# Optimization experiments

Hardware: AMD Instinct MI355X
Metric: run time of the kernel (lower is better)

Reference implementation:

```python
import jax, jax.numpy as jnp
import numpy as np

N_HEADS = 4
WINDOW = 606      # causal sliding-window width
K_PEEK = 606      # phy-output peek length (y_phy is zeros -> zeros anyway)
K_PEEK_TRUE = 30  # true-measurement peek length
LN_EPS = 1e-5


def _layernorm(x, g, b):
    m = jnp.mean(x, axis=-1, keepdims=True)
    v = jnp.var(x, axis=-1, keepdims=True)
    return (x - m) / jnp.sqrt(v + LN_EPS) * g + b


def _pos_encoding(T, d):
    pos = jnp.arange(T, dtype=jnp.float32)[:, None]
    div = jnp.exp(jnp.arange(0, d, 2, dtype=jnp.float32) * (-jnp.log(10000.0) / d))
    pe = jnp.zeros((T, d), jnp.float32)
    pe = pe.at[:, 0::2].set(jnp.sin(pos * div))
    pe = pe.at[:, 1::2].set(jnp.cos(pos * div))
    return pe


def setup_inputs() -> dict:
    key = jax.random.key(0)
    ks = iter(jax.random.split(key, 40))
    B, T, u_dim, y_dim, z_dim, h, L = 4, 2048, 8, 8, 16, 512, 4
    dff = 4 * h
    w = lambda shape: jax.random.normal(next(ks), shape, jnp.float32) * 0.02
    return {
        'u': jax.random.normal(next(ks), (B, u_dim, T), jnp.float32),
        'y': jax.random.normal(next(ks), (B, y_dim, T), jnp.float32),
        'W_in': w((u_dim + 2 * y_dim, h)), 'b_in': jnp.zeros((h,), jnp.float32),
        'qkv_w': w((L, h, 3 * h)), 'qkv_b': jnp.zeros((L, 3 * h), jnp.float32),
        'out_w': w((L, h, h)), 'out_b': jnp.zeros((L, h), jnp.float32),
        'ff1_w': w((L, h, dff)), 'ff1_b': jnp.zeros((L, dff), jnp.float32),
        'ff2_w': w((L, dff, h)), 'ff2_b': jnp.zeros((L, h), jnp.float32),
        'ln1_g': jnp.ones((L, h), jnp.float32), 'ln1_b': jnp.zeros((L, h), jnp.float32),
        'ln2_g': jnp.ones((L, h), jnp.float32), 'ln2_b': jnp.zeros((L, h), jnp.float32),
        'lnf_g': jnp.ones((h,), jnp.float32), 'lnf_b': jnp.zeros((h,), jnp.float32),
        'xm1_w': w((h, h)), 'xm1_b': jnp.zeros((h,), jnp.float32),
        'xm2_w': w((h, z_dim)), 'xm2_b': jnp.zeros((z_dim,), jnp.float32),
        'me1_w': w((z_dim, h)), 'me1_b': jnp.zeros((h,), jnp.float32),
        'me2_w': w((h, h)), 'me2_b': jnp.zeros((h,), jnp.float32),
        'me3_w': w((h, y_dim)), 'me3_b': jnp.zeros((y_dim,), jnp.float32),
    }


def _forward(u, y, W_in, b_in, qkv_w, qkv_b, out_w, out_b, ff1_w, ff1_b,
             ff2_w, ff2_b, ln1_g, ln1_b, ln2_g, ln2_b, lnf_g, lnf_b,
             xm1_w, xm1_b, xm2_w, xm2_b, me1_w, me1_b, me2_w, me2_b, me3_w, me3_b):
    B, y_dim, T = y.shape
    u_t = jnp.transpose(u, (0, 2, 1))          # [B,T,u_dim]
    y_t = jnp.transpose(y, (0, 2, 1))          # [B,T,y_dim]
    # phy rollout produces zeros (zero-init MODEL_PHY surrogate) -> y_aug = 0
    y_aug = jnp.zeros((B, T, y_dim), jnp.float32)
    k_true = min(K_PEEK_TRUE, T)
    y_aug_true = jnp.concatenate(
        [y_t[:, :k_true, :], jnp.zeros((B, T - k_true, y_dim), jnp.float32)], axis=1)
    u_aug = jnp.concatenate([u_t, y_aug, y_aug_true], axis=2)  # [B,T,u+2y]

    h = W_in.shape[1]
    x = u_aug @ W_in + b_in + _pos_encoding(T, h)[None]        # [B,T,h]

    # causal sliding-window mask: row i attends to j in [i-WINDOW+1, i]
    i = jnp.arange(T)[:, None]
    j = jnp.arange(T)[None, :]
    allowed = (j <= i) & (j > i - WINDOW)                      # [T,T] bool

    dh = h // N_HEADS
    L = qkv_w.shape[0]
    for l in range(L):
        qkv = x @ qkv_w[l] + qkv_b[l]                          # [B,T,3h]
        q, k, v = jnp.split(qkv, 3, axis=-1)
        q = q.reshape(B, T, N_HEADS, dh)
        k = k.reshape(B, T, N_HEADS, dh)
        v = v.reshape(B, T, N_HEADS, dh)
        scores = jnp.einsum('bqhd,bkhd->bhqk', q, k) / jnp.sqrt(jnp.float32(dh))
        scores = jnp.where(allowed[None, None], scores, jnp.float32(-1e30))
        probs = jax.nn.softmax(scores, axis=-1)
        attn = jnp.einsum('bhqk,bkhd->bqhd', probs, v).reshape(B, T, h)
        attn = attn @ out_w[l] + out_b[l]
        x = _layernorm(x + attn, ln1_g[l], ln1_b[l])           # post-norm
        ff = jax.nn.gelu(x @ ff1_w[l] + ff1_b[l], approximate=False) @ ff2_w[l] + ff2_b[l]
        x = _layernorm(x + ff, ln2_g[l], ln2_b[l])
    x = _layernorm(x, lnf_g, lnf_b)

    x_mean = jax.nn.gelu(x @ xm1_w + xm1_b, approximate=False) @ xm2_w + xm2_b
    hme = jax.nn.gelu(x_mean @ me1_w + me1_b, approximate=False)
    hme = jax.nn.gelu(hme @ me2_w + me2_b, approximate=False)
    y_hat = hme @ me3_w + me3_b                                # [B,T,y_dim]

    loss = jnp.sum((y_hat - y_t) ** 2)                         # lamba_smooth = 0
    return loss


def reference(u, y, W_in, b_in, qkv_w, qkv_b, out_w, out_b, ff1_w, ff1_b,
              ff2_w, ff2_b, ln1_g, ln1_b, ln2_g, ln2_b, lnf_g, lnf_b,
              xm1_w, xm1_b, xm2_w, xm2_b, me1_w, me1_b, me2_w, me2_b, me3_w, me3_b):
    return _forward(u, y, W_in, b_in, qkv_w, qkv_b, out_w, out_b, ff1_w, ff1_b,
                    ff2_w, ff2_b, ln1_g, ln1_b, ln2_g, ln2_b, lnf_g, lnf_b,
                    xm1_w, xm1_b, xm2_w, xm2_b, me1_w, me1_b, me2_w, me2_b, me3_w, me3_b)
```

## Files before the change

### kernel.cpp

```cpp
#include <hip/hip_runtime.h>
#include <cstdint>
#include <cstddef>

#define TT 2048
#define BB 4
#define HDIM 512
#define NH 4
#define LAYERS 4
#define WINDOW 606

#define PLANE_QK 4194304ull
#define PLANE_X  4194304ull
#define PLANE_FF 16777216ull

typedef __attribute__((ext_vector_type(8))) short bf16x8s;
typedef __attribute__((ext_vector_type(4))) float f32x4;

__device__ __forceinline__ float wred_sum(float v) {
#pragma unroll
  for (int off = 32; off; off >>= 1) v += __shfl_xor(v, off, 64);
  return v;
}
__device__ __forceinline__ float gelu_exact(float x) {
  return 0.5f * x * (1.0f + erff(x * 0.70710678118654752f));
}
__device__ __forceinline__ ushort bf16_rne(float v) {
  uint32_t u = __float_as_uint(v);
  u += 0x7FFFu + ((u >> 16) & 1u);
  return (ushort)(u >> 16);
}
__device__ __forceinline__ void split3(float v, ushort& h, ushort& l) {
  h = bf16_rne(v);
  const float hf = __uint_as_float(((uint32_t)h) << 16);
  l = bf16_rne(v - hf);
}
__device__ __forceinline__ void gld_lds16(const void* g, void* l) {
  __builtin_amdgcn_global_load_lds(
      (const __attribute__((address_space(1))) uint32_t*)g,
      (__attribute__((address_space(3))) uint32_t*)l, 16, 0, 0);
}

__global__ __launch_bounds__(256) void embed_kernel(
    const float* __restrict__ u, const float* __restrict__ y,
    const float* __restrict__ W_in, const float* __restrict__ b_in,
    float* __restrict__ X, ushort* __restrict__ xp) {
  const int row = blockIdx.x;
  const int b = row >> 11;
  const int t = row & 2047;
  const int tid = threadIdx.x;
  __shared__ float ua[24];
  if (tid < 8)       ua[tid] = u[((b << 3) + tid) * TT + t];
  else if (tid < 16) ua[tid] = 0.0f;
  else if (tid < 24) ua[tid] = (t < 30) ? y[((b << 3) + (tid - 16)) * TT + t] : 0.0f;
  __syncthreads();
#pragma unroll
  for (int c0 = 0; c0 < 2; ++c0) {
    const int c = c0 * 256 + tid;
    float s = b_in[c];
#pragma unroll
    for (int k = 0; k < 24; ++k) s += ua[k] * W_in[k * HDIM + c];
    const float dv = expf(-0.0179889460337f * (float)(c & ~1));
    const float arg = (float)t * dv;
    s += (c & 1) ? cosf(arg) : sinf(arg);
    X[(size_t)row * HDIM + c] = s;
    ushort h, l2; split3(s, h, l2);
    xp[(size_t)row * HDIM + c] = h;
    xp[PLANE_X + (size_t)row * HDIM + c] = l2;
  }
}

__device__ __forceinline__ void pack_tile(float (*tile)[33],
    const float* __restrict__ W, ushort* __restrict__ Wp,
    int K, int N, int bk, int bn, int tid) {
  const int i0 = tid >> 5, j = tid & 31;
#pragma unroll
  for (int i = 0; i < 4; ++i) {
    const int kk = i0 + i * 8;
    tile[kk][j] = W[(size_t)(bk + kk) * N + bn + j];
  }
  __syncthreads();
  const size_t NK = (size_t)N * K;
#pragma unroll
  for (int i = 0; i < 4; ++i) {
    const int nn = i0 + i * 8;
    const float v = tile[j][nn];
    ushort h, l2; split3(v, h, l2);
    ushort* base = Wp + (size_t)(bn + nn) * K + bk + j;
    base[0] = h; base[NK] = l2;
  }
}

__global__ __launch_bounds__(256) void packL_kernel(
    const float* __restrict__ qkvw, const float* __restrict__ outw,
    const float* __restrict__ ff1w, ushort* __restrict__ Wp) {
  __shared__ float tile[32][33];
  int i = blockIdx.x;
  if (i < 768) {
    pack_tile(tile, qkvw, Wp, 512, 1536, (i & 15) * 32, (i >> 4) * 32, threadIdx.x);
  } else if (i < 1024) {
    i -= 768;
    pack_tile(tile, outw, Wp + 1572864, 512, 512, (i & 15) * 32, (i >> 4) * 32, threadIdx.x);
  } else {
    i -= 1024;
    pack_tile(tile, ff1w, Wp + 2097152, 512, 2048, (i & 15) * 32, (i >> 4) * 32, threadIdx.x);
  }
}

__global__ __launch_bounds__(256) void packF_kernel(
    const float* __restrict__ ff2w, ushort* __restrict__ Wp) {
  __shared__ float tile[32][33];
  const int i = blockIdx.x;
  pack_tile(tile, ff2w, Wp, 2048, 512, (i & 63) * 32, (i >> 6) * 32, threadIdx.x);
}

__global__ __launch_bounds__(256) void packH_kernel(
    const float* __restrict__ xm1w, const float* __restrict__ me2w,
    ushort* __restrict__ Wp) {
  __shared__ float tile[32][33];
  int i = blockIdx.x;
  if (i < 256) pack_tile(tile, xm1w, Wp, 512, 512, (i & 15) * 32, (i >> 4) * 32, threadIdx.x);
  else { i -= 256; pack_tile(tile, me2w, Wp + 524288, 512, 512, (i & 15) * 32, (i >> 4) * 32, threadIdx.x); }
}

template <int ACT, int OUTMODE, int RM>
__global__ __launch_bounds__(256) void gemm_mfma(
    const ushort* __restrict__ Ah, const ushort* __restrict__ Al,
    const ushort* __restrict__ Bh, const ushort* __restrict__ Bl,
    const float* __restrict__ bias,
    float* __restrict__ C, ushort* __restrict__ Cp, size_t cplane,
    ushort* __restrict__ Wq, int M, int N, int K, int nbn) {
  constexpr int IA = RM / 32;
  constexpr int JA = RM / 64;
  __shared__ ushort AlsH[RM * 32];
  __shared__ ushort AlsL[RM * 32];
  __shared__ ushort BlsH[4096];
  __shared__ ushort BlsL[4096];
  __shared__ float biasL[128];
  const int tid = threadIdx.x;
  const int cpx = (int)gridDim.x >> 3;
  const int bid = blockIdx.x;
  const int lid = (bid & 7) * cpx + (bid >> 3);
  const int bn = (lid % nbn) * 128;
  const int bm = (lid / nbn) * RM;
  const int w = tid >> 6, ln = tid & 63;
  const int wr = (w >> 1) * (RM / 2), wc = (w & 1) * 64;
  const int c = ln & 15, g = ln >> 4;
  if (tid < 128) biasL[tid] = bias[bn + tid];
  const int srow = tid >> 2;
  const int scol = (tid & 3) * 8;

  f32x4 acc[IA][4] = {};
  for (int k0 = 0; k0 < K; k0 += 32) {
#pragma unroll
    for (int j = 0; j < JA; ++j) {
      const size_t ga = (size_t)(bm + j * 64 + srow) * K + k0 + scol;
      const int off = j * 4096 + tid * 16;
      gld_lds16(Ah + ga, (char*)AlsH + off);
      gld_lds16(Al + ga, (char*)AlsL + off);
    }
#pragma unroll
    for (int j = 0; j < 2; ++j) {
      const size_t gb = (size_t)(bn + j * 64 + srow) * K + k0 + scol;
      const int off = j * 4096 + tid * 16;
      gld_lds16(Bh + gb, (char*)BlsH + off);
      gld_lds16(Bl + gb, (char*)BlsL + off);
    }
    __syncthreads();
    bf16x8s fah[IA], fal[IA], fbh[4], fbl[4];
#pragma unroll
    for (int i = 0; i < IA; ++i) {
      const int ao = (wr + i * 16 + c) * 32 + g * 8;
      fah[i] = *(const bf16x8s*)&AlsH[ao];
      fal[i] = *(const bf16x8s*)&AlsL[ao];
    }
#pragma unroll
    for (int i = 0; i < 4; ++i) {
      const int bo = (wc + i * 16 + c) * 32 + g * 8;
      fbh[i] = *(const bf16x8s*)&BlsH[bo];
      fbl[i] = *(const bf16x8s*)&BlsL[bo];
    }
#pragma unroll
    for (int i = 0; i < IA; ++i)
#pragma unroll
      for (int j = 0; j < 4; ++j) {
        acc[i][j] = __builtin_amdgcn_mfma_f32_16x16x32_bf16(fah[i], fbh[j], acc[i][j], 0, 0, 0);
        acc[i][j] = __builtin_amdgcn_mfma_f32_16x16x32_bf16(fal[i], fbh[j], acc[i][j], 0, 0, 0);
        acc[i][j] = __builtin_amdgcn_mfma_f32_16x16x32_bf16(fah[i], fbl[j], acc[i][j], 0, 0, 0);
      }
    __syncthreads();
  }
  const float qscale = 0.08838834764831845f * 1.44269504088896341f;
#pragma unroll
  for (int i = 0; i < IA; ++i) {
    const int grow0 = bm + wr + i * 16 + g * 4;
#pragma unroll
    for (int j = 0; j < 4; ++j) {
      const int gcol = bn + wc + j * 16 + c;
      const float bv = biasL[wc + j * 16 + c];
      if (OUTMODE == 2) {
        const int bq = grow0 >> 11, tl = grow0 & 2047;
        if (bn < 512) {
          const int hh = gcol >> 7, d = gcol & 127;
          ushort* dst = Wq + ((size_t)(bq * NH + hh) * TT + tl) * 128 + d;
#pragma unroll
          for (int r = 0; r < 4; ++r) {
            ushort h, l2; split3((acc[i][j][r] + bv) * qscale, h, l2);
            dst[(size_t)r * 128] = h;
            dst[PLANE_QK + (size_t)r * 128] = l2;
          }
        } else if (bn < 1024) {
          const int hh = (gcol - 512) >> 7, d = gcol & 127;
          ushort* dst = Wq + 2 * PLANE_QK + ((size_t)(bq * NH + hh) * TT + tl) * 128 + d;
#pragma unroll
          for (int r = 0; r < 4; ++r) {
            ushort h, l2; split3(acc[i][j][r] + bv, h, l2);
            dst[(size_t)r * 128] = h;
            dst[PLANE_QK + (size_t)r * 128] = l2;
          }
        } else {
          const int hh = (gcol - 1024) >> 7, d = gcol & 127;
          ushort4 h4, l4;
          split3(acc[i][j][0] + bv, h4.x, l4.x);
          split3(acc[i][j][1] + bv, h4.y, l4.y);
          split3(acc[i][j][2] + bv, h4.z, l4.z);
          split3(acc[i][j][3] + bv, h4.w, l4.w);
          ushort* dst = Wq + 4 * PLANE_QK + ((size_t)(bq * NH + hh) * 128 + d) * TT + tl;
          *(ushort4*)dst = h4;
          *(ushort4*)(dst + PLANE_QK) = l4;
        }
      } else {
#pragma unroll
        for (int r = 0; r < 4; ++r) {
          float v = acc[i][j][r] + bv;
          if (ACT) v = gelu_exact(v);
          if (OUTMODE == 1) {
            ushort h, l2; split3(v, h, l2);
            ushort* base = Cp + (size_t)(grow0 + r) * N + gcol;
            base[0] = h; base[cplane] = l2;
          } else {
            C[(size_t)(grow0 + r) * N + gcol] = v;
          }
        }
      }
    }
  }
}

template <int ACT, int PACK>
__global__ __launch_bounds__(256) void gemm_bias(
    const float* __restrict__ A, const float* __restrict__ B,
    const float* __restrict__ bias, float* __restrict__ C,
    ushort* __restrict__ Cp, size_t cplane, int M, int N, int K) {
  __shared__ float As[16][132];
  __shared__ float Bs[16][64];
  const int bm = blockIdx.y * 128;
  const int bn = blockIdx.x * 64;
  const int tid = threadIdx.x;
  const int tx = tid & 15, ty = tid >> 4;
  float acc[8][4] = {};
  for (int k0 = 0; k0 < K; k0 += 16) {
#pragma unroll
    for (int i = 0; i < 8; ++i) {
      const int idx = i * 256 + tid;
      const int m = idx >> 4, k = idx & 15;
      As[k][m] = A[(size_t)(bm + m) * K + k0 + k];
    }
#pragma unroll
    for (int i = 0; i < 4; ++i) {
      const int idx = i * 256 + tid;
      const int k = idx >> 6, n = idx & 63;
      Bs[k][n] = (bn + n < N) ? B[(size_t)(k0 + k) * N + bn + n] : 0.0f;
    }
    __syncthreads();
#pragma unroll
    for (int kk = 0; kk < 16; ++kk) {
      float a[8], bb[4];
#pragma unroll
      for (int i = 0; i < 8; ++i) a[i] = As[kk][ty * 8 + i];
#pragma unroll
      for (int j = 0; j < 4; ++j) bb[j] = Bs[kk][tx * 4 + j];
#pragma unroll
      for (int i = 0; i < 8; ++i)
#pragma unroll
        for (int j = 0; j < 4; ++j) acc[i][j] += a[i] * bb[j];
    }
    __syncthreads();
  }
#pragma unroll
  for (int i = 0; i < 8; ++i) {
    const int m = bm + ty * 8 + i;
#pragma unroll
    for (int j = 0; j < 4; ++j) {
      const int n = bn + tx * 4 + j;
      if (n < N) {
        float v = acc[i][j] + bias[n];
        if (ACT) v = gelu_exact(v);
        if (PACK) {
          ushort h, l2; split3(v, h, l2);
          ushort* base = Cp + (size_t)m * N + n;
          base[0] = h; base[cplane] = l2;
        } else {
          C[(size_t)m * N + n] = v;
        }
      }
    }
  }
}

__global__ __launch_bounds__(256) void attn_mfma(
    const ushort* __restrict__ QKVp, ushort* __restrict__ atp) {
  const int bid = blockIdx.x;
  const int lid = (bid & 7) * 128 + (bid >> 3);
  const int q0 = (lid & 63) * 32;
  const int bh = lid >> 6;
  const int b = bh >> 2, hh = bh & 3;
  const int tid = threadIdx.x;
  const int w = tid >> 6, lane = tid & 63;
  const int c = lane & 15, g = lane >> 4;
  const int wr = w >> 1, wc = w & 1;

  __shared__ ushort Ph[32][40], Pl[32][40];
  __shared__ float wmax[2][32], wsum[2][32];
  __shared__ float mrow[2][32], lrow[2][32];

  const ushort* Qh = QKVp;
  const ushort* Ql = QKVp + PLANE_QK;
  const ushort* Kh = QKVp + 2 * PLANE_QK;
  const ushort* Kl = QKVp + 3 * PLANE_QK;
  const ushort* Vh = QKVp + 4 * PLANE_QK;
  const ushort* Vl = QKVp + 5 * PLANE_QK;

  const size_t qkbase = (size_t)bh * TT * 128;
  const size_t vtbase = (size_t)bh * 128 * TT;

  bf16x8s qh[4], ql[4];
  {
    const ushort* qr = Qh + qkbase + (size_t)(q0 + wr * 16 + c) * 128 + g * 8;
    const ushort* qr2 = Ql + qkbase + (size_t)(q0 + wr * 16 + c) * 128 + g * 8;
#pragma unroll
    for (int kc = 0; kc < 4; ++kc) {
      qh[kc] = *(const bf16x8s*)(qr + kc * 32);
      ql[kc] = *(const bf16x8s*)(qr2 + kc * 32);
    }
  }

  if (tid < 32) { mrow[0][tid] = -1e30f; lrow[0][tid] = 0.0f; }
  __syncthreads();

  f32x4 oacc[2][2] = {};
  int par = 0;
  int lo_ = q0 - (WINDOW - 1); if (lo_ < 0) lo_ = 0;
  const int k_first = lo_ & ~31;
  const int qg = q0 + wr * 16 + c;
  const int qrow = wr * 16 + c;

  for (int k0 = k_first; k0 <= q0; k0 += 32) {
    const bf16x8s vh0 = *(const bf16x8s*)(Vh + vtbase + (size_t)(w * 32 + c) * TT + k0 + g * 8);
    const bf16x8s vh1 = *(const bf16x8s*)(Vh + vtbase + (size_t)(w * 32 + 16 + c) * TT + k0 + g * 8);
    const bf16x8s vl0 = *(const bf16x8s*)(Vl + vtbase + (size_t)(w * 32 + c) * TT + k0 + g * 8);
    const bf16x8s vl1 = *(const bf16x8s*)(Vl + vtbase + (size_t)(w * 32 + 16 + c) * TT + k0 + g * 8);

    f32x4 sacc = {};
    {
      const ushort* kr = Kh + qkbase + (size_t)(k0 + wc * 16 + c) * 128 + g * 8;
      const ushort* kr2 = Kl + qkbase + (size_t)(k0 + wc * 16 + c) * 128 + g * 8;
      bf16x8s kh[4], kl[4];
#pragma unroll
      for (int kc = 0; kc < 4; ++kc) {
        kh[kc] = *(const bf16x8s*)(kr + kc * 32);
        kl[kc] = *(const bf16x8s*)(kr2 + kc * 32);
      }
#pragma unroll
      for (int kc = 0; kc < 4; ++kc)
        sacc = __builtin_amdgcn_mfma_f32_16x16x32_bf16(kh[kc], qh[kc], sacc, 0, 0, 0);
#pragma unroll
      for (int kc = 0; kc < 4; ++kc)
        sacc = __builtin_amdgcn_mfma_f32_16x16x32_bf16(kl[kc], qh[kc], sacc, 0, 0, 0);
#pragma unroll
      for (int kc = 0; kc < 4; ++kc)
        sacc = __builtin_amdgcn_mfma_f32_16x16x32_bf16(kh[kc], ql[kc], sacc, 0, 0, 0);
    }
    float s[4];
    float m4 = -1e30f;
#pragma unroll
    for (int r = 0; r < 4; ++r) {
      const int kj = k0 + wc * 16 + g * 4 + r;
      const bool ok = (kj <= qg) && (kj > qg - WINDOW);
      s[r] = ok ? sacc[r] : -1e30f;
      m4 = fmaxf(m4, s[r]);
    }
    m4 = fmaxf(m4, __shfl_xor(m4, 16, 64));
    m4 = fmaxf(m4, __shfl_xor(m4, 32, 64));
    if (lane < 16) wmax[wc][qrow] = m4;
    __syncthreads();

    {
      const float mt = fmaxf(wmax[0][qrow], wmax[1][qrow]);
      const float mn = fmaxf(mrow[par][qrow], mt);
      float pv[4];
      float ps = 0.0f;
#pragma unroll
      for (int r = 0; r < 4; ++r) {
        pv[r] = (s[r] > -1e29f) ? exp2f(s[r] - mn) : 0.0f;
        ps += pv[r];
      }
      ps += __shfl_xor(ps, 16, 64);
      ps += __shfl_xor(ps, 32, 64);
      if (lane < 16) wsum[wc][qrow] = ps;
      ushort4 h4, l4;
      split3(pv[0], h4.x, l4.x); split3(pv[1], h4.y, l4.y);
      split3(pv[2], h4.z, l4.z); split3(pv[3], h4.w, l4.w);
      *(ushort4*)&Ph[qrow][wc * 16 + g * 4] = h4;
      *(ushort4*)&Pl[qrow][wc * 16 + g * 4] = l4;
    }
    __syncthreads();

    if (tid < 32) {
      const float mt = fmaxf(wmax[0][tid], wmax[1][tid]);
      const float mo = mrow[par][tid];
      const float mn = fmaxf(mo, mt);
      mrow[par ^ 1][tid] = mn;
      lrow[par ^ 1][tid] = lrow[par][tid] * exp2f(mo - mn) + wsum[0][tid] + wsum[1][tid];
    }
#pragma unroll
    for (int rh = 0; rh < 2; ++rh) {
      float sc[4];
#pragma unroll
      for (int r = 0; r < 4; ++r) {
        const int row = rh * 16 + g * 4 + r;
        const float mt = fmaxf(wmax[0][row], wmax[1][row]);
        const float mo = mrow[par][row];
        sc[r] = exp2f(mo - fmaxf(mo, mt));
      }
#pragma unroll
      for (int jt = 0; jt < 2; ++jt)
#pragma unroll
        for (int r = 0; r < 4; ++r) oacc[rh][jt][r] *= sc[r];
      const bf16x8s pah = *(const bf16x8s*)&Ph[rh * 16 + c][g * 8];
      const bf16x8s pal = *(const bf16x8s*)&Pl[rh * 16 + c][g * 8];
      oacc[rh][0] = __builtin_amdgcn_mfma_f32_16x16x32_bf16(pah, vh0, oacc[rh][0], 0, 0, 0);
      oacc[rh][0] = __builtin_amdgcn_mfma_f32_16x16x32_bf16(pal, vh0, oacc[rh][0], 0, 0, 0);
      oacc[rh][0] = __builtin_amdgcn_mfma_f32_16x16x32_bf16(pah, vl0, oacc[rh][0], 0, 0, 0);
      oacc[rh][1] = __builtin_amdgcn_mfma_f32_16x16x32_bf16(pah, vh1, oacc[rh][1], 0, 0, 0);
      oacc[rh][1] = __builtin_amdgcn_mfma_f32_16x16x32_bf16(pal, vh1, oacc[rh][1], 0, 0, 0);
      oacc[rh][1] = __builtin_amdgcn_mfma_f32_16x16x32_bf16(pah, vl1, oacc[rh][1], 0, 0, 0);
    }
    __syncthreads();
    par ^= 1;
  }

#pragma unroll
  for (int rh = 0; rh < 2; ++rh) {
#pragma unroll
    for (int r = 0; r < 4; ++r) {
      const int row = rh * 16 + g * 4 + r;
      const float li = 1.0f / lrow[par][row];
      const int qgo = q0 + row;
      ushort* base = atp + (size_t)(b * TT + qgo) * HDIM + hh * 128;
#pragma unroll
      for (int jt = 0; jt < 2; ++jt) {
        const int d = w * 32 + jt * 16 + c;
        ushort h, l2; split3(oacc[rh][jt][r] * li, h, l2);
        base[d] = h;
        base[PLANE_X + d] = l2;
      }
    }
  }
}

template <int HAS_RES>
__global__ __launch_bounds__(128) void ln_kernel(
    const float* __restrict__ x, const float* __restrict__ r,
    const float* __restrict__ g, const float* __restrict__ be,
    float* __restrict__ out, ushort* __restrict__ xp) {
  const int row = blockIdx.x, tid = threadIdx.x;
  float4 v = ((const float4*)(x + (size_t)row * HDIM))[tid];
  if (HAS_RES) {
    const float4 rv = ((const float4*)(r + (size_t)row * HDIM))[tid];
    v.x += rv.x; v.y += rv.y; v.z += rv.z; v.w += rv.w;
  }
  __shared__ float red[2];
  float s = v.x + v.y + v.z + v.w;
  s = wred_sum(s);
  if ((tid & 63) == 0) red[tid >> 6] = s;
  __syncthreads();
  const float mean = (red[0] + red[1]) * (1.0f / 512.0f);
  const float dx = v.x - mean, dy = v.y - mean, dz = v.z - mean, dw = v.w - mean;
  float s2 = dx * dx + dy * dy + dz * dz + dw * dw;
  __syncthreads();
  s2 = wred_sum(s2);
  if ((tid & 63) == 0) red[tid >> 6] = s2;
  __syncthreads();
  const float var = (red[0] + red[1]) * (1.0f / 512.0f);
  const float inv = 1.0f / sqrtf(var + 1e-5f);
  const float4 gv = ((const float4*)g)[tid];
  const float4 bv = ((const float4*)be)[tid];
  float4 o;
  o.x = dx * inv * gv.x + bv.x;
  o.y = dy * inv * gv.y + bv.y;
  o.z = dz * inv * gv.z + bv.z;
  o.w = dw * inv * gv.w + bv.w;
  ((float4*)(out + (size_t)row * HDIM))[tid] = o;
  ushort4 h4, l4;
  split3(o.x, h4.x, l4.x); split3(o.y, h4.y, l4.y);
  split3(o.z, h4.z, l4.z); split3(o.w, h4.w, l4.w);
  ushort* basep = xp + (size_t)row * HDIM + tid * 4;
  *(ushort4*)basep = h4;
  *(ushort4*)(basep + PLANE_X) = l4;
}

__global__ __launch_bounds__(256) void head_loss_kernel(
    const float* __restrict__ hme, const float* __restrict__ w3,
    const float* __restrict__ b3, const float* __restrict__ y,
    float* __restrict__ partials) {
  const int row = blockIdx.x;
  const int b = row >> 11, t = row & 2047;
  const int tid = threadIdx.x;
  __shared__ __align__(16) float hl[512];
  __shared__ float acc8[8];
  ((float2*)hl)[tid] = ((const float2*)(hme + (size_t)row * HDIM))[tid];
  __syncthreads();
  const int d = tid >> 5, l32 = tid & 31;
  float s = 0.0f;
  for (int k = l32; k < 512; k += 32) s += hl[k] * w3[k * 8 + d];
#pragma unroll
  for (int off = 16; off; off >>= 1) s += __shfl_xor(s, off, 64);
  if (l32 == 0) {
    const float yh = s + b3[d];
    const float diff = yh - y[((b << 3) + d) * TT + t];
    acc8[d] = diff * diff;
  }
  __syncthreads();
  if (tid == 0) {
    float tot = 0.0f;
#pragma unroll
    for (int i = 0; i < 8; ++i) tot += acc8[i];
    partials[row] = tot;
  }
}

__global__ __launch_bounds__(256) void reduce_kernel(
    const float* __restrict__ partials, float* __restrict__ out, int n) {
  float s = 0.0f;
  for (int i = threadIdx.x; i < n; i += 256) s += partials[i];
  s = wred_sum(s);
  __shared__ float red[4];
  if ((threadIdx.x & 63) == 0) red[threadIdx.x >> 6] = s;
  __syncthreads();
  if (threadIdx.x == 0) out[0] = red[0] + red[1] + red[2] + red[3];
}

extern "C" void kernel_launch(void* const* d_in, const int* in_sizes, int n_in,
                              void* d_out, int out_size, void* d_ws, size_t ws_size,
                              hipStream_t stream) {
  (void)in_sizes; (void)n_in; (void)out_size; (void)ws_size;
  const float* u     = (const float*)d_in[0];
  const float* y     = (const float*)d_in[1];
  const float* W_in  = (const float*)d_in[2];
  const float* b_in  = (const float*)d_in[3];
  const float* qkv_w = (const float*)d_in[4];
  const float* qkv_b = (const float*)d_in[5];
  const float* out_w = (const float*)d_in[6];
  const float* out_b = (const float*)d_in[7];
  const float* ff1_w = (const float*)d_in[8];
  const float* ff1_b = (const float*)d_in[9];
  const float* ff2_w = (const float*)d_in[10];
  const float* ff2_b = (const float*)d_in[11];
  const float* ln1_g = (const float*)d_in[12];
  const float* ln1_b = (const float*)d_in[13];
  const float* ln2_g = (const float*)d_in[14];
  const float* ln2_b = (const float*)d_in[15];
  const float* lnf_g = (const float*)d_in[16];
  const float* lnf_b = (const float*)d_in[17];
  const float* xm1_w = (const float*)d_in[18];
  const float* xm1_b = (const float*)d_in[19];
  const float* xm2_w = (const float*)d_in[20];
  const float* xm2_b = (const float*)d_in[21];
  const float* me1_w = (const float*)d_in[22];
  const float* me1_b = (const float*)d_in[23];
  const float* me2_w = (const float*)d_in[24];
  const float* me2_b = (const float*)d_in[25];
  const float* me3_w = (const float*)d_in[26];
  const float* me3_b = (const float*)d_in[27];

  const int M = BB * TT;
  char* ws = (char*)d_ws;
  float*  X    = (float*)(ws);
  float*  PRJ  = (float*)(ws + ((size_t)16 << 20));
  ushort* BIGp = (ushort*)(ws + ((size_t)32 << 20));
  ushort* PK1  = (ushort*)(ws + ((size_t)96 << 20));
  ushort* WSCR = (ushort*)(ws + ((size_t)112 << 20));
  float*  XM   = (float*)(ws + ((size_t)120 << 20));
  float*  PART = (float*)(ws + ((size_t)121 << 20));

  embed_kernel<<<M, 256, 0, stream>>>(u, y, W_in, b_in, X, PK1);

  for (int l = 0; l < LAYERS; ++l) {
    packL_kernel<<<2048, 256, 0, stream>>>(
        qkv_w + (size_t)l * 512 * 1536, out_w + (size_t)l * 512 * 512,
        ff1_w + (size_t)l * 512 * 2048, WSCR);
    gemm_mfma<0, 2, 128><<<768, 256, 0, stream>>>(
        PK1, PK1 + PLANE_X, WSCR, WSCR + 786432, qkv_b + l * 1536,
        nullptr, nullptr, 0, BIGp, M, 1536, 512, 12);
    attn_mfma<<<1024, 256, 0, stream>>>(BIGp, PK1);
    gemm_mfma<0, 0, 64><<<512, 256, 0, stream>>>(
        PK1, PK1 + PLANE_X, WSCR + 1572864, WSCR + 1835008, out_b + l * 512,
        PRJ, nullptr, 0, nullptr, M, 512, 512, 4);
    ln_kernel<1><<<M, 128, 0, stream>>>(X, PRJ, ln1_g + l * 512, ln1_b + l * 512, X, PK1);
    gemm_mfma<1, 1, 128><<<1024, 256, 0, stream>>>(
        PK1, PK1 + PLANE_X, WSCR + 2097152, WSCR + 3145728, ff1_b + l * 2048,
        nullptr, BIGp, PLANE_FF, nullptr, M, 2048, 512, 16);
    packF_kernel<<<1024, 256, 0, stream>>>(ff2_w + (size_t)l * 2048 * 512, WSCR);
    gemm_mfma<0, 0, 64><<<512, 256, 0, stream>>>(
        BIGp, BIGp + PLANE_FF, WSCR, WSCR + 1048576, ff2_b + l * 512,
        PRJ, nullptr, 0, nullptr, M, 512, 2048, 4);
    ln_kernel<1><<<M, 128, 0, stream>>>(X, PRJ, ln2_g + l * 512, ln2_b + l * 512, X, PK1);
  }
  ln_kernel<0><<<M, 128, 0, stream>>>(X, nullptr, lnf_g, lnf_b, X, PK1);

  packH_kernel<<<512, 256, 0, stream>>>(xm1_w, me2_w, WSCR);
  gemm_mfma<1, 0, 64><<<512, 256, 0, stream>>>(
      PK1, PK1 + PLANE_X, WSCR, WSCR + 262144, xm1_b,
      PRJ, nullptr, 0, nullptr, M, 512, 512, 4);
  gemm_bias<0, 0><<<dim3(1, 64), 256, 0, stream>>>(PRJ, xm2_w, xm2_b, XM, nullptr, 0, M, 16, 512);
  gemm_bias<1, 1><<<dim3(8, 64), 256, 0, stream>>>(XM, me1_w, me1_b, nullptr, PK1, PLANE_X, M, 512, 16);
  gemm_mfma<1, 0, 64><<<512, 256, 0, stream>>>(
      PK1, PK1 + PLANE_X, WSCR + 524288, WSCR + 786432, me2_b,
      PRJ, nullptr, 0, nullptr, M, 512, 512, 4);
  head_loss_kernel<<<M, 256, 0, stream>>>(PRJ, me3_w, me3_b, y, PART);
  reduce_kernel<<<1, 256, 0, stream>>>(PART, (float*)d_out, M);
}
```

Measured before the change: 1.854 ms.

## Process 64 keys per attention iteration and raise MFMA wave priority

The sliding-window attention loop now handles 64 keys per step instead of 32. It computes two score tiles side by side and widens the shared P buffers to 64 columns. This halves the number of per-iteration __syncthreads barriers and online-softmax rescale passes, and gives more independent MFMA chains to interleave. It also wraps the MFMA sections in s_setprio. The cost is higher register pressure and some extra masked work at window edges, since the start is now aligned to 64.

```diff
diff --git a/kernel.cpp b/kernel.cpp
--- a/kernel.cpp
+++ b/kernel.cpp
@@ -319,7 +319,7 @@
   const int c = lane & 15, g = lane >> 4;
   const int wr = w >> 1, wc = w & 1;
 
-  __shared__ ushort Ph[32][40], Pl[32][40];
+  __shared__ ushort Ph[32][72], Pl[32][72];
   __shared__ float wmax[2][32], wsum[2][32];
   __shared__ float mrow[2][32], lrow[2][32];
 
@@ -350,68 +350,92 @@
   f32x4 oacc[2][2] = {};
   int par = 0;
   int lo_ = q0 - (WINDOW - 1); if (lo_ < 0) lo_ = 0;
-  const int k_first = lo_ & ~31;
+  const int k_first = lo_ & ~63;
   const int qg = q0 + wr * 16 + c;
   const int qrow = wr * 16 + c;
 
-  for (int k0 = k_first; k0 <= q0; k0 += 32) {
-    const bf16x8s vh0 = *(const bf16x8s*)(Vh + vtbase + (size_t)(w * 32 + c) * TT + k0 + g * 8);
-    const bf16x8s vh1 = *(const bf16x8s*)(Vh + vtbase + (size_t)(w * 32 + 16 + c) * TT + k0 + g * 8);
-    const bf16x8s vl0 = *(const bf16x8s*)(Vl + vtbase + (size_t)(w * 32 + c) * TT + k0 + g * 8);
-    const bf16x8s vl1 = *(const bf16x8s*)(Vl + vtbase + (size_t)(w * 32 + 16 + c) * TT + k0 + g * 8);
-
-    f32x4 sacc = {};
+  for (int k0 = k_first; k0 < q0 + 32; k0 += 64) {
+    f32x4 sA = {}, sB = {};
     {
-      const ushort* kr = Kh + qkbase + (size_t)(k0 + wc * 16 + c) * 128 + g * 8;
-      const ushort* kr2 = Kl + qkbase + (size_t)(k0 + wc * 16 + c) * 128 + g * 8;
-      bf16x8s kh[4], kl[4];
+      const ushort* krA  = Kh + qkbase + (size_t)(k0 + wc * 16 + c) * 128 + g * 8;
+      const ushort* krA2 = Kl + qkbase + (size_t)(k0 + wc * 16 + c) * 128 + g * 8;
+      const ushort* krB  = Kh + qkbase + (size_t)(k0 + 32 + wc * 16 + c) * 128 + g * 8;
+      const ushort* krB2 = Kl + qkbase + (size_t)(k0 + 32 + wc * 16 + c) * 128 + g * 8;
+      bf16x8s kAh[4], kAl[4], kBh[4], kBl[4];
 #pragma unroll
       for (int kc = 0; kc < 4; ++kc) {
-        kh[kc] = *(const bf16x8s*)(kr + kc * 32);
-        kl[kc] = *(const bf16x8s*)(kr2 + kc * 32);
-      }
-#pragma unroll
-      for (int kc = 0; kc < 4; ++kc)
-        sacc = __builtin_amdgcn_mfma_f32_16x16x32_bf16(kh[kc], qh[kc], sacc, 0, 0, 0);
-#pragma unroll
-      for (int kc = 0; kc < 4; ++kc)
-        sacc = __builtin_amdgcn_mfma_f32_16x16x32_bf16(kl[kc], qh[kc], sacc, 0, 0, 0);
-#pragma unroll
-      for (int kc = 0; kc < 4; ++kc)
-        sacc = __builtin_amdgcn_mfma_f32_16x16x32_bf16(kh[kc], ql[kc], sacc, 0, 0, 0);
-    }
-    float s[4];
-    float m4 = -1e30f;
+        kAh[kc] = *(const bf16x8s*)(krA + kc * 32);
+        kAl[kc] = *(const bf16x8s*)(krA2 + kc * 32);
+        kBh[kc] = *(const bf16x8s*)(krB + kc * 32);
+        kBl[kc] = *(const bf16x8s*)(krB2 + kc * 32);
+      }
+      __builtin_amdgcn_s_setprio(1);
+#pragma unroll
+      for (int kc = 0; kc < 4; ++kc) {
+        sA = __builtin_amdgcn_mfma_f32_16x16x32_bf16(kAh[kc], qh[kc], sA, 0, 0, 0);
+        sB = __builtin_amdgcn_mfma_f32_16x16x32_bf16(kBh[kc], qh[kc], sB, 0, 0, 0);
+      }
+#pragma unroll
+      for (int kc = 0; kc < 4; ++kc) {
+        sA = __builtin_amdgcn_mfma_f32_16x16x32_bf16(kAl[kc], qh[kc], sA, 0, 0, 0);
+        sB = __builtin_amdgcn_mfma_f32_16x16x32_bf16(kBl[kc], qh[kc], sB, 0, 0, 0);
+      }
+#pragma unroll
+      for (int kc = 0; kc < 4; ++kc) {
+        sA = __builtin_amdgcn_mfma_f32_16x16x32_bf16(kAh[kc], ql[kc], sA, 0, 0, 0);
+        sB = __builtin_amdgcn_mfma_f32_16x16x32_bf16(kBh[kc], ql[kc], sB, 0, 0, 0);
+      }
+      __builtin_amdgcn_s_setprio(0);
+    }
+
+    bf16x8s vfh[2][2], vfl[2][2];
+#pragma unroll
+    for (int kh2 = 0; kh2 < 2; ++kh2)
+#pragma unroll
+      for (int jt = 0; jt < 2; ++jt) {
+        const size_t voff = vtbase + (size_t)(w * 32 + jt * 16 + c) * TT + k0 + kh2 * 32 + g * 8;
+        vfh[kh2][jt] = *(const bf16x8s*)(Vh + voff);
+        vfl[kh2][jt] = *(const bf16x8s*)(Vl + voff);
+      }
+
+    float e[8];
+    float mx = -1e30f;
 #pragma unroll
     for (int r = 0; r < 4; ++r) {
-      const int kj = k0 + wc * 16 + g * 4 + r;
-      const bool ok = (kj <= qg) && (kj > qg - WINDOW);
-      s[r] = ok ? sacc[r] : -1e30f;
-      m4 = fmaxf(m4, s[r]);
-    }
-    m4 = fmaxf(m4, __shfl_xor(m4, 16, 64));
-    m4 = fmaxf(m4, __shfl_xor(m4, 32, 64));
-    if (lane < 16) wmax[wc][qrow] = m4;
+      const int kjA = k0 + wc * 16 + 4 * g + r;
+      const int kjB = kjA + 32;
+      const bool okA = (kjA <= qg) && (kjA > qg - WINDOW);
+      const bool okB = (kjB <= qg) && (kjB > qg - WINDOW);
+      e[r]     = okA ? sA[r] : -1e30f;
+      e[4 + r] = okB ? sB[r] : -1e30f;
+      mx = fmaxf(mx, fmaxf(e[r], e[4 + r]));
+    }
+    mx = fmaxf(mx, __shfl_xor(mx, 16, 64));
+    mx = fmaxf(mx, __shfl_xor(mx, 32, 64));
+    if (lane < 16) wmax[wc][qrow] = mx;
     __syncthreads();
 
     {
       const float mt = fmaxf(wmax[0][qrow], wmax[1][qrow]);
       const float mn = fmaxf(mrow[par][qrow], mt);
-      float pv[4];
       float ps = 0.0f;
 #pragma unroll
-      for (int r = 0; r < 4; ++r) {
-        pv[r] = (s[r] > -1e29f) ? exp2f(s[r] - mn) : 0.0f;
-        ps += pv[r];
+      for (int i = 0; i < 8; ++i) {
+        e[i] = (e[i] > -1e29f) ? exp2f(e[i] - mn) : 0.0f;
+        ps += e[i];
       }
       ps += __shfl_xor(ps, 16, 64);
       ps += __shfl_xor(ps, 32, 64);
       if (lane < 16) wsum[wc][qrow] = ps;
-      ushort4 h4, l4;
-      split3(pv[0], h4.x, l4.x); split3(pv[1], h4.y, l4.y);
-      split3(pv[2], h4.z, l4.z); split3(pv[3], h4.w, l4.w);
-      *(ushort4*)&Ph[qrow][wc * 16 + g * 4] = h4;
-      *(ushort4*)&Pl[qrow][wc * 16 + g * 4] = l4;
+      ushort4 hA, lA, hB, lB;
+      split3(e[0], hA.x, lA.x); split3(e[1], hA.y, lA.y);
+      split3(e[2], hA.z, lA.z); split3(e[3], hA.w, lA.w);
+      split3(e[4], hB.x, lB.x); split3(e[5], hB.y, lB.y);
+      split3(e[6], hB.z, lB.z); split3(e[7], hB.w, lB.w);
+      *(ushort4*)&Ph[qrow][wc * 16 + 4 * g] = hA;
+      *(ushort4*)&Pl[qrow][wc * 16 + 4 * g] = lA;
+      *(ushort4*)&Ph[qrow][32 + wc * 16 + 4 * g] = hB;
+      *(ushort4*)&Pl[qrow][32 + wc * 16 + 4 * g] = lB;
     }
     __syncthreads();
 
@@ -436,14 +460,19 @@
       for (int jt = 0; jt < 2; ++jt)
 #pragma unroll
         for (int r = 0; r < 4; ++r) oacc[rh][jt][r] *= sc[r];
-      const bf16x8s pah = *(const bf16x8s*)&Ph[rh * 16 + c][g * 8];
-      const bf16x8s pal = *(const bf16x8s*)&Pl[rh * 16 + c][g * 8];
-      oacc[rh][0] = __builtin_amdgcn_mfma_f32_16x16x32_bf16(pah, vh0, oacc[rh][0], 0, 0, 0);
-      oacc[rh][0] = __builtin_amdgcn_mfma_f32_16x16x32_bf16(pal, vh0, oacc[rh][0], 0, 0, 0);
-      oacc[rh][0] = __builtin_amdgcn_mfma_f32_16x16x32_bf16(pah, vl0, oacc[rh][0], 0, 0, 0);
-      oacc[rh][1] = __builtin_amdgcn_mfma_f32_16x16x32_bf16(pah, vh1, oacc[rh][1], 0, 0, 0);
-      oacc[rh][1] = __builtin_amdgcn_mfma_f32_16x16x32_bf16(pal, vh1, oacc[rh][1], 0, 0, 0);
-      oacc[rh][1] = __builtin_amdgcn_mfma_f32_16x16x32_bf16(pah, vl1, oacc[rh][1], 0, 0, 0);
+      __builtin_amdgcn_s_setprio(1);
+#pragma unroll
+      for (int kh2 = 0; kh2 < 2; ++kh2) {
+        const bf16x8s pah = *(const bf16x8s*)&Ph[rh * 16 + c][kh2 * 32 + g * 8];
+        const bf16x8s pal = *(const bf16x8s*)&Pl[rh * 16 + c][kh2 * 32 + g * 8];
+        oacc[rh][0] = __builtin_amdgcn_mfma_f32_16x16x32_bf16(pah, vfh[kh2][0], oacc[rh][0], 0, 0, 0);
+        oacc[rh][0] = __builtin_amdgcn_mfma_f32_16x16x32_bf16(pal, vfh[kh2][0], oacc[rh][0], 0, 0, 0);
+        oacc[rh][0] = __builtin_amdgcn_mfma_f32_16x16x32_bf16(pah, vfl[kh2][0], oacc[rh][0], 0, 0, 0);
+        oacc[rh][1] = __builtin_amdgcn_mfma_f32_16x16x32_bf16(pah, vfh[kh2][1], oacc[rh][1], 0, 0, 0);
+        oacc[rh][1] = __builtin_amdgcn_mfma_f32_16x16x32_bf16(pal, vfh[kh2][1], oacc[rh][1], 0, 0, 0);
+        oacc[rh][1] = __builtin_amdgcn_mfma_f32_16x16x32_bf16(pah, vfl[kh2][1], oacc[rh][1], 0, 0, 0);
+      }
+      __builtin_amdgcn_s_setprio(0);
     }
     __syncthreads();
     par ^= 1;
```

Measured after the change: 1.998 ms. +7.7%, slower.
